# Optimization experiments

Measured on AMD Instinct MI355X. Metric: run time of the kernel, lower is better.

## Reference

```python
import jax, jax.numpy as jnp
import numpy as np

VOCAB, EMB, H, LAYERS, B, T = 50000, 128, 128, 3, 64, 512


def _lstm_dir(x, w_ih, w_hh, b_ih, b_hh, h0, c0, reverse):
    # x: [B,T,Din]; w_ih: [4H,Din]; w_hh: [4H,H]; h0,c0: [B,H]
    xg = jnp.einsum('btd,gd->btg', x, w_ih) + b_ih + b_hh  # [B,T,4H]

    def step(carry, xg_t):
        h, c = carry
        g = xg_t + h @ w_hh.T  # [B,4H]
        i, f, gg, o = jnp.split(g, 4, axis=-1)  # torch gate order i,f,g,o
        c = jax.nn.sigmoid(f) * c + jax.nn.sigmoid(i) * jnp.tanh(gg)
        h = jax.nn.sigmoid(o) * jnp.tanh(c)
        return (h, c), h

    _, hs = jax.lax.scan(step, (h0, c0), jnp.swapaxes(xg, 0, 1), reverse=reverse)
    return jnp.swapaxes(hs, 0, 1)  # [B,T,H], aligned with input time order


def _bidir_layer(x, w_ih, w_hh, b_ih, b_hh, h0, c0):
    # stacked params: leading dim 2 = (fwd, bwd)
    fwd = _lstm_dir(x, w_ih[0], w_hh[0], b_ih[0], b_hh[0], h0[0], c0[0], False)
    bwd = _lstm_dir(x, w_ih[1], w_hh[1], b_ih[1], b_hh[1], h0[1], c0[1], True)
    return jnp.concatenate([fwd, bwd], axis=-1)  # [B,T,2H]


def setup_inputs() -> dict:
    key = jax.random.key(0)
    ks = jax.random.split(key, 20)
    s = 1.0 / np.sqrt(H)
    inp = {
        'X_batch': jax.random.randint(ks[0], (B, T), 0, VOCAB),
        'emb': jax.random.normal(ks[1], (VOCAB, EMB), jnp.float32),
        'hx': jax.random.normal(ks[2], (2 * LAYERS, B, H), jnp.float32),
        'cx': jax.random.normal(ks[3], (2 * LAYERS, B, H), jnp.float32),
        'lin_w': jax.random.uniform(ks[4], (1, 2 * H), jnp.float32, -s, s),
        'lin_b': jax.random.uniform(ks[5], (1,), jnp.float32, -s, s),
    }
    k = 6
    for l in range(LAYERS):
        din = EMB if l == 0 else 2 * H
        inp[f'w_ih_{l}'] = jax.random.uniform(ks[k], (2, 4 * H, din), jnp.float32, -s, s); k += 1
        inp[f'w_hh_{l}'] = jax.random.uniform(ks[k], (2, 4 * H, H), jnp.float32, -s, s); k += 1
        inp[f'b_ih_{l}'] = jax.random.uniform(ks[k], (2, 4 * H), jnp.float32, -s, s); k += 1
        inp[f'b_hh_{l}'] = jax.random.uniform(ks[k], (2, 4 * H), jnp.float32, -s, s); k += 1
    return inp


def reference(X_batch, emb, hx, cx, lin_w, lin_b,
              w_ih_0, w_hh_0, b_ih_0, b_hh_0,
              w_ih_1, w_hh_1, b_ih_1, b_hh_1,
              w_ih_2, w_hh_2, b_ih_2, b_hh_2):
    x = emb[X_batch]  # [B,T,EMB]
    params = [(w_ih_0, w_hh_0, b_ih_0, b_hh_0),
              (w_ih_1, w_hh_1, b_ih_1, b_hh_1),
              (w_ih_2, w_hh_2, b_ih_2, b_hh_2)]
    for l, (wi, wh, bi, bh) in enumerate(params):
        x = _bidir_layer(x, wi, wh, bi, bh, hx[2 * l:2 * l + 2], cx[2 * l:2 * l + 2])
    # linear head applied to last timestep (== output[:, -1] of full linear)
    return x[:, -1] @ lin_w.T + lin_b  # [B,1]
```

## Files before the change

kernel.cpp:

```cpp
#include <hip/hip_runtime.h>
#include <hip/hip_bf16.h>
#include <stdint.h>

#define B_    64
#define T_    512
#define EMB_  128
#define H_    128
#define G4    512
#define M_    (B_ * T_)

typedef __attribute__((ext_vector_type(8))) short     short8;
typedef __attribute__((ext_vector_type(4))) float     floatx4;
typedef __attribute__((ext_vector_type(2))) _Float16  half2v;

#define GLDS(g, l) __builtin_amdgcn_global_load_lds( \
    (__attribute__((address_space(1))) void*)(g),    \
    (__attribute__((address_space(3))) void*)(l), 16, 0, 0)

__device__ __forceinline__ unsigned short f2bf_bits(float f) {
  __hip_bfloat16 h = __float2bfloat16(f);
  return *reinterpret_cast<unsigned short*>(&h);
}
__device__ __forceinline__ float bf_bits2f(unsigned short u) {
  unsigned int x = ((unsigned int)u) << 16;
  return __uint_as_float(x);
}
__device__ __forceinline__ float sigm(float x) {
  return __fdividef(1.0f, 1.0f + __expf(-x));
}
__device__ __forceinline__ float tanh_fast(float x) {
  return 1.0f - __fdividef(2.0f, __expf(2.0f * x) + 1.0f);
}

__device__ __forceinline__ unsigned int pack_f16x2(float a, float b) {
  half2v h; h.x = (_Float16)a; h.y = (_Float16)b;
  return __builtin_bit_cast(unsigned int, h);
}
__device__ __forceinline__ half2v u2h2(unsigned int u) {
  return __builtin_bit_cast(half2v, u);
}

#if __has_builtin(__builtin_amdgcn_fdot2)
__device__ __forceinline__ float fdot2(half2v a, half2v b, float c) {
  return __builtin_amdgcn_fdot2(a, b, c, false);
}
#else
__device__ __forceinline__ float fdot2(half2v a, half2v b, float c) {
  return fmaf((float)a.x, (float)b.x, fmaf((float)a.y, (float)b.y, c));
}
#endif

__device__ __forceinline__ float quad_bfly_add(float x) {
  float y = x + __int_as_float(
      __builtin_amdgcn_mov_dpp(__float_as_int(x), 0xB1, 0xF, 0xF, true));
  return y + __int_as_float(
      __builtin_amdgcn_mov_dpp(__float_as_int(y), 0x4E, 0xF, 0xF, true));
}

__device__ __forceinline__ void barrier_lds_only() {
  __asm__ __volatile__("s_waitcnt lgkmcnt(0)\n\ts_barrier" ::: "memory");
}

__device__ __forceinline__ void  store_xg(float* p, float v)  { *p = v; }
__device__ __forceinline__ void  store_xg(unsigned short* p, float v) { *p = f2bf_bits(v); }
__device__ __forceinline__ float load_xg(const float* p)  { return *p; }
__device__ __forceinline__ float load_xg(const unsigned short* p) { return bf_bits2f(*p); }

__global__ void k_gather(const int* __restrict__ X, const float* __restrict__ emb,
                         unsigned short* __restrict__ x0) {
  int i = blockIdx.x * 256 + threadIdx.x;
  int row = i >> 5, c4 = i & 31;
  float4 v = ((const float4*)emb)[(size_t)X[row] * 32 + c4];
  ushort4 o;
  o.x = f2bf_bits(v.x); o.y = f2bf_bits(v.y); o.z = f2bf_bits(v.z); o.w = f2bf_bits(v.w);
  ((ushort4*)x0)[i] = o;
}

__global__ void k_prep(const float* __restrict__ w, const float* __restrict__ bi,
                       const float* __restrict__ bh, unsigned short* __restrict__ wb,
                       float* __restrict__ bias, int nw) {
  int i = blockIdx.x * blockDim.x + threadIdx.x;
  int stride = gridDim.x * blockDim.x;
  for (int k = i; k < nw; k += stride) wb[k] = f2bf_bits(w[k]);
  for (int k = i; k < 2 * G4; k += stride) bias[k] = bi[k] + bh[k];
}

__global__ void k_prep_whh(const float* __restrict__ Whh, unsigned int* __restrict__ wf) {
  int i = blockIdx.x * 256 + threadIdx.x;
  int dir = i >> 15;
  int t2  = i & 0x7FFF;
  int jq  = t2 >> 11;
  int t3  = t2 & 0x7FF;
  int ts  = t3 >> 2;
  int q   = t3 & 3;
  int d   = jq * 4 + q;
  int g   = d >> 4;
  int jj  = d & 15;
  int lane = ts & 63, wave = ts >> 6;
  int p = lane & 3, ul = lane >> 2;
  int u = wave * 16 + ul;
  int k = 32 * p + 2 * jj;
  const float* wr = Whh + ((size_t)dir * G4 + g * H_ + u) * H_ + k;
  wf[i] = pack_f16x2(wr[0], wr[1]);
}

template <typename XG_T>
__global__ __launch_bounds__(256, 2) void k_gemm(
    const unsigned short* __restrict__ A,
    const unsigned short* __restrict__ W,
    const float* __restrict__ bias,
    XG_T* __restrict__ xg,
    int K) {
  __shared__ unsigned short sA[128 * 32];
  __shared__ unsigned short sB[128 * 32];
  const int tid  = threadIdx.x;
  const int lane = tid & 63;
  const int wave = tid >> 6;
  const int mt = blockIdx.x, nt = blockIdx.y, dir = blockIdx.z;
  const size_t Arow0 = (size_t)mt * 128;
  const int    Ncol0 = nt * 128;
  const unsigned short* Wd = W + (size_t)dir * G4 * K;

  const int srow = tid >> 2;
  const int qlog = (tid & 3) ^ ((tid >> 4) & 3);
  auto ldsA0 = (__attribute__((address_space(3))) void*)(sA + wave * 512);
  auto ldsA1 = (__attribute__((address_space(3))) void*)(sA + 2048 + wave * 512);
  auto ldsB0 = (__attribute__((address_space(3))) void*)(sB + wave * 512);
  auto ldsB1 = (__attribute__((address_space(3))) void*)(sB + 2048 + wave * 512);

  floatx4 acc[4][4];
#pragma unroll
  for (int i = 0; i < 4; ++i)
#pragma unroll
    for (int j = 0; j < 4; ++j) acc[i][j] = (floatx4)0.0f;

  const int wrow = (wave >> 1) * 64, wcol = (wave & 1) * 64;
  const int frow = lane & 15;
  const int fq   = lane >> 4;

  for (int kt = 0; kt < K; kt += 32) {
    const unsigned short* gA0 = A  + (Arow0 + srow) * (size_t)K + kt + qlog * 8;
    const unsigned short* gB0 = Wd + (size_t)(Ncol0 + srow) * K + kt + qlog * 8;
    GLDS(gA0, ldsA0);
    GLDS(gA0 + (size_t)64 * K, ldsA1);
    GLDS(gB0, ldsB0);
    GLDS(gB0 + (size_t)64 * K, ldsB1);
    __syncthreads();

    short8 af[4], bf[4];
#pragma unroll
    for (int i = 0; i < 4; ++i) {
      int r  = wrow + 16 * i + frow;
      int rn = wcol + 16 * i + frow;
      af[i] = *(const short8*)(sA + r  * 32 + ((fq ^ ((r  >> 2) & 3)) * 8));
      bf[i] = *(const short8*)(sB + rn * 32 + ((fq ^ ((rn >> 2) & 3)) * 8));
    }
#pragma unroll
    for (int i = 0; i < 4; ++i)
#pragma unroll
      for (int j = 0; j < 4; ++j)
        acc[i][j] = __builtin_amdgcn_mfma_f32_16x16x32_bf16(af[i], bf[j], acc[i][j], 0, 0, 0);
    __syncthreads();
  }

  const int r0 = (lane >> 4) * 4;
  const int cc = lane & 15;
  XG_T* xgd = xg + (size_t)dir * M_ * G4;
#pragma unroll
  for (int j = 0; j < 4; ++j) {
    int gcol = Ncol0 + wcol + 16 * j + cc;
    float bs = bias[dir * G4 + gcol];
#pragma unroll
    for (int i = 0; i < 4; ++i) {
      size_t rowb = Arow0 + wrow + 16 * i + r0;
#pragma unroll
      for (int r = 0; r < 4; ++r)
        store_xg(&xgd[(rowb + r) * G4 + gcol], acc[i][j][r] + bs);
    }
  }
}

template <typename XG_T>
__global__ __attribute__((amdgpu_flat_work_group_size(512, 512),
                          amdgpu_waves_per_eu(2, 2))) void k_scan(
    const unsigned int* __restrict__ wf,
    const float* __restrict__ hx0,
    const float* __restrict__ cx0,
    const XG_T* __restrict__ xg,
    unsigned short* __restrict__ y)
{
  const int b   = blockIdx.x & 63;
  const int dir = blockIdx.x >> 6;
  const int tid = threadIdx.x;
  const int lane = tid & 63;
  const int wave = tid >> 6;
  const int p  = lane & 3;
  const int ul = lane >> 2;
  const int u  = wave * 16 + ul;

  __shared__ __align__(16) unsigned short h16[2][128];

  uint4 wv[16];
  const uint4* wfv = (const uint4*)wf;
#pragma unroll
  for (int i = 0; i < 16; ++i) wv[i] = wfv[(dir * 16 + i) * 512 + tid];

  float c = cx0[(size_t)dir * B_ * H_ + b * H_ + u];
  if (p == 0) {
    float h0 = hx0[(size_t)dir * B_ * H_ + b * H_ + u];
    h16[0][u] = (unsigned short)(pack_f16x2(h0, 0.0f) & 0xFFFF);
  }

  const XG_T* xgb = xg + ((size_t)dir * M_ + (size_t)b * T_) * G4;
  const intptr_t xstep = dir ? -(intptr_t)G4 : (intptr_t)G4;
  const XG_T* xrow0 = xgb + (dir ? (size_t)(T_ - 1) * G4 : 0) + p * H_ + u;
  float xp0 = load_xg(xrow0);
  float xp1 = load_xg(xrow0 + xstep);
  const XG_T* xld = xrow0 + 2 * xstep;

  unsigned short* yp = y + ((size_t)b * T_ + (dir ? T_ - 1 : 0)) * (2 * H_)
                         + dir * H_ + u;
  const intptr_t ystep = dir ? -(intptr_t)(2 * H_) : (intptr_t)(2 * H_);

  __syncthreads();

  auto dots = [&](int par, float xv, float& g0, float& g1, float& g2, float& g3) {
    const uint4* hv4 = (const uint4*)&h16[par][0];
    uint4 h0v = hv4[4 * p + 0], h1v = hv4[4 * p + 1];
    uint4 h2v = hv4[4 * p + 2], h3v = hv4[4 * p + 3];
    half2v hh[16] = {
      u2h2(h0v.x), u2h2(h0v.y), u2h2(h0v.z), u2h2(h0v.w),
      u2h2(h1v.x), u2h2(h1v.y), u2h2(h1v.z), u2h2(h1v.w),
      u2h2(h2v.x), u2h2(h2v.y), u2h2(h2v.z), u2h2(h2v.w),
      u2h2(h3v.x), u2h2(h3v.y), u2h2(h3v.z), u2h2(h3v.w)};
    g0 = 0; g1 = 0; g2 = 0; g3 = 0;
#pragma unroll
    for (int j = 0; j < 16; ++j) {
      g0 = fdot2(u2h2(((const unsigned int*)&wv[(0 * 16 + j) >> 2])[(0 * 16 + j) & 3]), hh[j], g0);
      g1 = fdot2(u2h2(((const unsigned int*)&wv[(1 * 16 + j) >> 2])[(1 * 16 + j) & 3]), hh[j], g1);
      g2 = fdot2(u2h2(((const unsigned int*)&wv[(2 * 16 + j) >> 2])[(2 * 16 + j) & 3]), hh[j], g2);
      g3 = fdot2(u2h2(((const unsigned int*)&wv[(3 * 16 + j) >> 2])[(3 * 16 + j) & 3]), hh[j], g3);
    }
    g0 += (p == 0) ? xv : 0.0f;
    g1 += (p == 1) ? xv : 0.0f;
    g2 += (p == 2) ? xv : 0.0f;
    g3 += (p == 3) ? xv : 0.0f;
  };

  auto finish = [&](int par, float g0, float g1, float g2, float g3) {
    g0 = quad_bfly_add(g0);
    g1 = quad_bfly_add(g1);
    g2 = quad_bfly_add(g2);
    g3 = quad_bfly_add(g3);
    float iv = sigm(g0), fv = sigm(g1), gv = tanh_fast(g2), ov = sigm(g3);
    c = fmaf(fv, c, iv * gv);
    float h = ov * tanh_fast(c);
    if (p == 0) {
      h16[par ^ 1][u] = (unsigned short)(pack_f16x2(h, 0.0f) & 0xFFFF);
      *yp = f2bf_bits(h);
    }
    yp += ystep;
    barrier_lds_only();
  };

  for (int t = 0; t < T_; t += 2) {
    float a0, a1, a2, a3;
    dots(0, xp0, a0, a1, a2, a3);
    xp0 = (t + 2 < T_) ? load_xg(xld) : 0.0f;
    xld += xstep;
    finish(0, a0, a1, a2, a3);
    dots(1, xp1, a0, a1, a2, a3);
    xp1 = (t + 3 < T_) ? load_xg(xld) : 0.0f;
    xld += xstep;
    finish(1, a0, a1, a2, a3);
  }
}

__global__ void k_head(const unsigned short* __restrict__ y2, const float* __restrict__ lw,
                       const float* __restrict__ lb, float* __restrict__ out) {
  int b = blockIdx.x, l = threadIdx.x;
  const unsigned short* row = y2 + ((size_t)b * T_ + (T_ - 1)) * (2 * H_);
  float s = 0;
#pragma unroll
  for (int k = 0; k < 4; ++k) s += bf_bits2f(row[l + 64 * k]) * lw[l + 64 * k];
#pragma unroll
  for (int off = 32; off > 0; off >>= 1) s += __shfl_down(s, off);
  if (l == 0) out[b] = s + lb[0];
}

template <typename XG_T>
static inline void run_layers(const unsigned int* const* wfs,
                              const unsigned short* x0,
                              unsigned short* y0, unsigned short* y1, unsigned short* y2,
                              const unsigned short* wb0, const unsigned short* wb1,
                              const unsigned short* wb2,
                              const float* bias0, const float* bias1, const float* bias2,
                              const float* hx, const float* cx,
                              XG_T* xg, hipStream_t stream) {
  dim3 gg(M_ / 128, G4 / 128, 2);
  k_gemm<XG_T><<<gg, 256, 0, stream>>>(x0, wb0, bias0, xg, EMB_);
  k_scan<XG_T><<<128, 512, 0, stream>>>(wfs[0], hx, cx, xg, y0);
  k_gemm<XG_T><<<gg, 256, 0, stream>>>(y0, wb1, bias1, xg, 2 * H_);
  k_scan<XG_T><<<128, 512, 0, stream>>>(wfs[1], hx + 2 * B_ * H_, cx + 2 * B_ * H_, xg, y1);
  k_gemm<XG_T><<<gg, 256, 0, stream>>>(y1, wb2, bias2, xg, 2 * H_);
  k_scan<XG_T><<<128, 512, 0, stream>>>(wfs[2], hx + 4 * B_ * H_, cx + 4 * B_ * H_, xg, y2);
}

extern "C" void kernel_launch(void* const* d_in, const int* in_sizes, int n_in,
                              void* d_out, int out_size, void* d_ws, size_t ws_size,
                              hipStream_t stream) {
  const int*   X   = (const int*)d_in[0];
  const float* emb = (const float*)d_in[1];
  const float* hx  = (const float*)d_in[2];
  const float* cx  = (const float*)d_in[3];
  const float* lw  = (const float*)d_in[4];
  const float* lb  = (const float*)d_in[5];
  const float* w_ih[3] = {(const float*)d_in[6],  (const float*)d_in[10], (const float*)d_in[14]};
  const float* w_hh[3] = {(const float*)d_in[7],  (const float*)d_in[11], (const float*)d_in[15]};
  const float* b_ih[3] = {(const float*)d_in[8],  (const float*)d_in[12], (const float*)d_in[16]};
  const float* b_hh[3] = {(const float*)d_in[9],  (const float*)d_in[13], (const float*)d_in[17]};
  float* out = (float*)d_out;

  char* ws = (char*)d_ws;
  size_t off = 0;
  auto carve = [&](size_t bytes) {
    char* p = ws + off;
    off = (off + bytes + 255) & ~(size_t)255;
    return p;
  };
  unsigned short* x0  = (unsigned short*)carve((size_t)M_ * EMB_ * 2);
  unsigned short* y0  = (unsigned short*)carve((size_t)M_ * 2 * H_ * 2);
  unsigned short* y1  = (unsigned short*)carve((size_t)M_ * 2 * H_ * 2);
  unsigned short* y2  = (unsigned short*)carve((size_t)M_ * 2 * H_ * 2);
  unsigned short* wb0 = (unsigned short*)carve((size_t)2 * G4 * EMB_ * 2);
  unsigned short* wb1 = (unsigned short*)carve((size_t)2 * G4 * 2 * H_ * 2);
  unsigned short* wb2 = (unsigned short*)carve((size_t)2 * G4 * 2 * H_ * 2);
  float* bias0 = (float*)carve(2 * G4 * 4);
  float* bias1 = (float*)carve(2 * G4 * 4);
  float* bias2 = (float*)carve(2 * G4 * 4);
  unsigned int* wf0 = (unsigned int*)carve((size_t)65536 * 4);
  unsigned int* wf1 = (unsigned int*)carve((size_t)65536 * 4);
  unsigned int* wf2 = (unsigned int*)carve((size_t)65536 * 4);
  const size_t xg_f32_bytes = (size_t)2 * M_ * G4 * 4;
  const bool use_f32 = (off + xg_f32_bytes) <= ws_size;
  void* xg = carve(use_f32 ? xg_f32_bytes : xg_f32_bytes / 2);

  k_prep<<<256, 256, 0, stream>>>(w_ih[0], b_ih[0], b_hh[0], wb0, bias0, 2 * G4 * EMB_);
  k_prep<<<256, 256, 0, stream>>>(w_ih[1], b_ih[1], b_hh[1], wb1, bias1, 2 * G4 * 2 * H_);
  k_prep<<<256, 256, 0, stream>>>(w_ih[2], b_ih[2], b_hh[2], wb2, bias2, 2 * G4 * 2 * H_);
  k_prep_whh<<<256, 256, 0, stream>>>(w_hh[0], wf0);
  k_prep_whh<<<256, 256, 0, stream>>>(w_hh[1], wf1);
  k_prep_whh<<<256, 256, 0, stream>>>(w_hh[2], wf2);
  k_gather<<<(M_ * 32) / 256, 256, 0, stream>>>(X, emb, x0);

  const unsigned int* wfs[3] = {wf0, wf1, wf2};
  if (use_f32)
    run_layers<float>(wfs, x0, y0, y1, y2, wb0, wb1, wb2, bias0, bias1, bias2,
                      hx, cx, (float*)xg, stream);
  else
    run_layers<unsigned short>(wfs, x0, y0, y1, y2, wb0, wb1, wb2, bias0, bias1, bias2,
                               hx, cx, (unsigned short*)xg, stream);

  k_head<<<64, 64, 0, stream>>>(y2, lw, lb, out);
}
```

Measured before the change: 1.333 ms.

## Split recurrent dot products across lane pairs with 256-thread scan blocks

The LSTM scan kernel now uses 256 threads per block, with each hidden unit handled by 2 lanes instead of 4. Each lane keeps twice as many recurrent weights in registers (32 uint4). The cross-lane reduction drops from two DPP steps to one, and dual accumulators shorten the fdot2 dependency chains. The aim is to cut per-timestep reduction and barrier cost across fewer waves, at the price of higher register pressure and more serial work per lane; the weight repacking kernel is updated to match.

```diff
diff --git a/kernel.cpp b/kernel.cpp
--- a/kernel.cpp
+++ b/kernel.cpp
@@ -50,15 +50,14 @@
 }
 #endif
 
-__device__ __forceinline__ float quad_bfly_add(float x) {
-  float y = x + __int_as_float(
+__device__ __forceinline__ float pair_bfly_add(float x) {
+  return x + __int_as_float(
       __builtin_amdgcn_mov_dpp(__float_as_int(x), 0xB1, 0xF, 0xF, true));
-  return y + __int_as_float(
-      __builtin_amdgcn_mov_dpp(__float_as_int(y), 0x4E, 0xF, 0xF, true));
 }
 
 __device__ __forceinline__ void barrier_lds_only() {
-  __asm__ __volatile__("s_waitcnt lgkmcnt(0)\n\ts_barrier" ::: "memory");
+  __builtin_amdgcn_s_waitcnt(0xC07F);
+  __builtin_amdgcn_s_barrier();
 }
 
 __device__ __forceinline__ void  store_xg(float* p, float v)  { *p = v; }
@@ -88,18 +87,18 @@
 __global__ void k_prep_whh(const float* __restrict__ Whh, unsigned int* __restrict__ wf) {
   int i = blockIdx.x * 256 + threadIdx.x;
   int dir = i >> 15;
-  int t2  = i & 0x7FFF;
-  int jq  = t2 >> 11;
-  int t3  = t2 & 0x7FF;
-  int ts  = t3 >> 2;
-  int q   = t3 & 3;
-  int d   = jq * 4 + q;
-  int g   = d >> 4;
-  int jj  = d & 15;
-  int lane = ts & 63, wave = ts >> 6;
-  int p = lane & 3, ul = lane >> 2;
-  int u = wave * 16 + ul;
-  int k = 32 * p + 2 * jj;
+  int r   = i & 0x7FFF;
+  int i4  = r >> 10;
+  int r2  = r & 0x3FF;
+  int ts  = r2 >> 2;
+  int q   = r2 & 3;
+  int d   = i4 * 4 + q;
+  int g   = d >> 5;
+  int jj  = d & 31;
+  int lane = ts & 63, w = ts >> 6;
+  int p = lane & 1, ul = lane >> 1;
+  int u = w * 32 + ul;
+  int k = 64 * p + 2 * jj;
   const float* wr = Whh + ((size_t)dir * G4 + g * H_ + u) * H_ + k;
   wf[i] = pack_f16x2(wr[0], wr[1]);
 }
@@ -181,8 +180,8 @@
 }
 
 template <typename XG_T>
-__global__ __attribute__((amdgpu_flat_work_group_size(512, 512),
-                          amdgpu_waves_per_eu(2, 2))) void k_scan(
+__global__ __attribute__((amdgpu_flat_work_group_size(256, 256),
+                          amdgpu_waves_per_eu(1, 1))) void k_scan(
     const unsigned int* __restrict__ wf,
     const float* __restrict__ hx0,
     const float* __restrict__ cx0,
@@ -194,16 +193,16 @@
   const int tid = threadIdx.x;
   const int lane = tid & 63;
   const int wave = tid >> 6;
-  const int p  = lane & 3;
-  const int ul = lane >> 2;
-  const int u  = wave * 16 + ul;
+  const int p  = lane & 1;
+  const int ul = lane >> 1;
+  const int u  = wave * 32 + ul;
 
   __shared__ __align__(16) unsigned short h16[2][128];
 
-  uint4 wv[16];
+  uint4 wv[32];
   const uint4* wfv = (const uint4*)wf;
 #pragma unroll
-  for (int i = 0; i < 16; ++i) wv[i] = wfv[(dir * 16 + i) * 512 + tid];
+  for (int i = 0; i < 32; ++i) wv[i] = wfv[(dir * 32 + i) * 256 + tid];
 
   float c = cx0[(size_t)dir * B_ * H_ + b * H_ + u];
   if (p == 0) {
@@ -213,9 +212,11 @@
 
   const XG_T* xgb = xg + ((size_t)dir * M_ + (size_t)b * T_) * G4;
   const intptr_t xstep = dir ? -(intptr_t)G4 : (intptr_t)G4;
-  const XG_T* xrow0 = xgb + (dir ? (size_t)(T_ - 1) * G4 : 0) + p * H_ + u;
-  float xp0 = load_xg(xrow0);
-  float xp1 = load_xg(xrow0 + xstep);
+  const int o0 = (2 * p) * H_ + u;
+  const int o1 = o0 + H_;
+  const XG_T* xrow0 = xgb + (dir ? (size_t)(T_ - 1) * G4 : 0);
+  float xa0 = load_xg(xrow0 + o0), xb0 = load_xg(xrow0 + o1);
+  float xa1 = load_xg(xrow0 + xstep + o0), xb1 = load_xg(xrow0 + xstep + o1);
   const XG_T* xld = xrow0 + 2 * xstep;
 
   unsigned short* yp = y + ((size_t)b * T_ + (dir ? T_ - 1 : 0)) * (2 * H_)
@@ -224,34 +225,45 @@
 
   __syncthreads();
 
-  auto dots = [&](int par, float xv, float& g0, float& g1, float& g2, float& g3) {
+  auto dots = [&](int par, float xva, float xvb,
+                  float& g0, float& g1, float& g2, float& g3) {
     const uint4* hv4 = (const uint4*)&h16[par][0];
-    uint4 h0v = hv4[4 * p + 0], h1v = hv4[4 * p + 1];
-    uint4 h2v = hv4[4 * p + 2], h3v = hv4[4 * p + 3];
-    half2v hh[16] = {
-      u2h2(h0v.x), u2h2(h0v.y), u2h2(h0v.z), u2h2(h0v.w),
-      u2h2(h1v.x), u2h2(h1v.y), u2h2(h1v.z), u2h2(h1v.w),
-      u2h2(h2v.x), u2h2(h2v.y), u2h2(h2v.z), u2h2(h2v.w),
-      u2h2(h3v.x), u2h2(h3v.y), u2h2(h3v.z), u2h2(h3v.w)};
-    g0 = 0; g1 = 0; g2 = 0; g3 = 0;
+    uint4 hq[8];
+#pragma unroll
+    for (int i = 0; i < 8; ++i) hq[i] = hv4[8 * p + i];
+    half2v hh[32];
+#pragma unroll
+    for (int i = 0; i < 8; ++i) {
+      hh[4 * i + 0] = u2h2(hq[i].x);
+      hh[4 * i + 1] = u2h2(hq[i].y);
+      hh[4 * i + 2] = u2h2(hq[i].z);
+      hh[4 * i + 3] = u2h2(hq[i].w);
+    }
+    float A0 = 0, B0 = 0, A1 = 0, B1 = 0, A2 = 0, B2 = 0, A3 = 0, B3 = 0;
 #pragma unroll
     for (int j = 0; j < 16; ++j) {
-      g0 = fdot2(u2h2(((const unsigned int*)&wv[(0 * 16 + j) >> 2])[(0 * 16 + j) & 3]), hh[j], g0);
-      g1 = fdot2(u2h2(((const unsigned int*)&wv[(1 * 16 + j) >> 2])[(1 * 16 + j) & 3]), hh[j], g1);
-      g2 = fdot2(u2h2(((const unsigned int*)&wv[(2 * 16 + j) >> 2])[(2 * 16 + j) & 3]), hh[j], g2);
-      g3 = fdot2(u2h2(((const unsigned int*)&wv[(3 * 16 + j) >> 2])[(3 * 16 + j) & 3]), hh[j], g3);
-    }
-    g0 += (p == 0) ? xv : 0.0f;
-    g1 += (p == 1) ? xv : 0.0f;
-    g2 += (p == 2) ? xv : 0.0f;
-    g3 += (p == 3) ? xv : 0.0f;
+      int d0 = j, d1 = j + 16;
+      A0 = fdot2(u2h2(((const unsigned int*)&wv[(0 * 32 + d0) >> 2])[(0 * 32 + d0) & 3]), hh[d0], A0);
+      A1 = fdot2(u2h2(((const unsigned int*)&wv[(1 * 32 + d0) >> 2])[(1 * 32 + d0) & 3]), hh[d0], A1);
+      A2 = fdot2(u2h2(((const unsigned int*)&wv[(2 * 32 + d0) >> 2])[(2 * 32 + d0) & 3]), hh[d0], A2);
+      A3 = fdot2(u2h2(((const unsigned int*)&wv[(3 * 32 + d0) >> 2])[(3 * 32 + d0) & 3]), hh[d0], A3);
+      B0 = fdot2(u2h2(((const unsigned int*)&wv[(0 * 32 + d1) >> 2])[(0 * 32 + d1) & 3]), hh[d1], B0);
+      B1 = fdot2(u2h2(((const unsigned int*)&wv[(1 * 32 + d1) >> 2])[(1 * 32 + d1) & 3]), hh[d1], B1);
+      B2 = fdot2(u2h2(((const unsigned int*)&wv[(2 * 32 + d1) >> 2])[(2 * 32 + d1) & 3]), hh[d1], B2);
+      B3 = fdot2(u2h2(((const unsigned int*)&wv[(3 * 32 + d1) >> 2])[(3 * 32 + d1) & 3]), hh[d1], B3);
+    }
+    g0 = A0 + B0; g1 = A1 + B1; g2 = A2 + B2; g3 = A3 + B3;
+    g0 += (p == 0) ? xva : 0.0f;
+    g1 += (p == 0) ? xvb : 0.0f;
+    g2 += (p == 1) ? xva : 0.0f;
+    g3 += (p == 1) ? xvb : 0.0f;
   };
 
   auto finish = [&](int par, float g0, float g1, float g2, float g3) {
-    g0 = quad_bfly_add(g0);
-    g1 = quad_bfly_add(g1);
-    g2 = quad_bfly_add(g2);
-    g3 = quad_bfly_add(g3);
+    g0 = pair_bfly_add(g0);
+    g1 = pair_bfly_add(g1);
+    g2 = pair_bfly_add(g2);
+    g3 = pair_bfly_add(g3);
     float iv = sigm(g0), fv = sigm(g1), gv = tanh_fast(g2), ov = sigm(g3);
     c = fmaf(fv, c, iv * gv);
     float h = ov * tanh_fast(c);
@@ -264,15 +276,24 @@
   };
 
   for (int t = 0; t < T_; t += 2) {
-    float a0, a1, a2, a3;
-    dots(0, xp0, a0, a1, a2, a3);
-    xp0 = (t + 2 < T_) ? load_xg(xld) : 0.0f;
-    xld += xstep;
-    finish(0, a0, a1, a2, a3);
-    dots(1, xp1, a0, a1, a2, a3);
-    xp1 = (t + 3 < T_) ? load_xg(xld) : 0.0f;
-    xld += xstep;
-    finish(1, a0, a1, a2, a3);
+    {
+      float va = xa0, vb = xb0;
+      if (t + 2 < T_) { xa0 = load_xg(xld + o0); xb0 = load_xg(xld + o1); }
+      else            { xa0 = 0.0f; xb0 = 0.0f; }
+      xld += xstep;
+      float a0, a1, a2, a3;
+      dots(0, va, vb, a0, a1, a2, a3);
+      finish(0, a0, a1, a2, a3);
+    }
+    {
+      float va = xa1, vb = xb1;
+      if (t + 3 < T_) { xa1 = load_xg(xld + o0); xb1 = load_xg(xld + o1); }
+      else            { xa1 = 0.0f; xb1 = 0.0f; }
+      xld += xstep;
+      float a0, a1, a2, a3;
+      dots(1, va, vb, a0, a1, a2, a3);
+      finish(1, a0, a1, a2, a3);
+    }
   }
 }
 
@@ -299,11 +320,11 @@
                               XG_T* xg, hipStream_t stream) {
   dim3 gg(M_ / 128, G4 / 128, 2);
   k_gemm<XG_T><<<gg, 256, 0, stream>>>(x0, wb0, bias0, xg, EMB_);
-  k_scan<XG_T><<<128, 512, 0, stream>>>(wfs[0], hx, cx, xg, y0);
+  k_scan<XG_T><<<128, 256, 0, stream>>>(wfs[0], hx, cx, xg, y0);
   k_gemm<XG_T><<<gg, 256, 0, stream>>>(y0, wb1, bias1, xg, 2 * H_);
-  k_scan<XG_T><<<128, 512, 0, stream>>>(wfs[1], hx + 2 * B_ * H_, cx + 2 * B_ * H_, xg, y1);
+  k_scan<XG_T><<<128, 256, 0, stream>>>(wfs[1], hx + 2 * B_ * H_, cx + 2 * B_ * H_, xg, y1);
   k_gemm<XG_T><<<gg, 256, 0, stream>>>(y1, wb2, bias2, xg, 2 * H_);
-  k_scan<XG_T><<<128, 512, 0, stream>>>(wfs[2], hx + 4 * B_ * H_, cx + 4 * B_ * H_, xg, y2);
+  k_scan<XG_T><<<128, 256, 0, stream>>>(wfs[2], hx + 4 * B_ * H_, cx + 4 * B_ * H_, xg, y2);
 }
 
 extern "C" void kernel_launch(void* const* d_in, const int* in_sizes, int n_in,
```

Result: faster. 1.121 ms (-15.9%).

## Halve scan workgroup to 4 waves, each thread computing two hidden units

Applied to the files above, without the earlier changes.

The recurrent scan kernel now runs with 256 threads instead of 512. Each thread holds twice as many W_hh fragments in registers (32 uint4) and computes dot products for two hidden units, and the quad lanes pick their own unit's gates after the butterfly reduction. The W_hh repacking kernel is changed to match the new layout. The aim is a cheaper per-step barrier with fewer waves and more independent FMA chains per thread, at the cost of doubling dot-product work per thread and higher register pressure. The barrier inline asm is also swapped for builtins.

```diff
diff --git a/kernel.cpp b/kernel.cpp
--- a/kernel.cpp
+++ b/kernel.cpp
@@ -58,7 +58,8 @@
 }
 
 __device__ __forceinline__ void barrier_lds_only() {
-  __asm__ __volatile__("s_waitcnt lgkmcnt(0)\n\ts_barrier" ::: "memory");
+  __builtin_amdgcn_s_waitcnt(0xC07F);
+  __builtin_amdgcn_s_barrier();
 }
 
 __device__ __forceinline__ void  store_xg(float* p, float v)  { *p = v; }
@@ -88,17 +89,18 @@
 __global__ void k_prep_whh(const float* __restrict__ Whh, unsigned int* __restrict__ wf) {
   int i = blockIdx.x * 256 + threadIdx.x;
   int dir = i >> 15;
-  int t2  = i & 0x7FFF;
-  int jq  = t2 >> 11;
-  int t3  = t2 & 0x7FF;
-  int ts  = t3 >> 2;
-  int q   = t3 & 3;
-  int d   = jq * 4 + q;
-  int g   = d >> 4;
+  int r   = i & 0x7FFF;
+  int i4  = r >> 10;
+  int r2  = r & 0x3FF;
+  int ts  = r2 >> 2;
+  int qq  = r2 & 3;
+  int d   = i4 * 4 + qq;
+  int U   = d >> 6;
+  int g   = (d >> 4) & 3;
   int jj  = d & 15;
-  int lane = ts & 63, wave = ts >> 6;
-  int p = lane & 3, ul = lane >> 2;
-  int u = wave * 16 + ul;
+  int lane = ts & 63, w = ts >> 6;
+  int p = lane & 3, q = lane >> 2;
+  int u = w * 32 + U * 16 + q;
   int k = 32 * p + 2 * jj;
   const float* wr = Whh + ((size_t)dir * G4 + g * H_ + u) * H_ + k;
   wf[i] = pack_f16x2(wr[0], wr[1]);
@@ -181,8 +183,8 @@
 }
 
 template <typename XG_T>
-__global__ __attribute__((amdgpu_flat_work_group_size(512, 512),
-                          amdgpu_waves_per_eu(2, 2))) void k_scan(
+__global__ __attribute__((amdgpu_flat_work_group_size(256, 256),
+                          amdgpu_waves_per_eu(1, 1))) void k_scan(
     const unsigned int* __restrict__ wf,
     const float* __restrict__ hx0,
     const float* __restrict__ cx0,
@@ -195,27 +197,30 @@
   const int lane = tid & 63;
   const int wave = tid >> 6;
   const int p  = lane & 3;
-  const int ul = lane >> 2;
-  const int u  = wave * 16 + ul;
+  const int q  = lane >> 2;
+  const int uA = wave * 32 + q;
+  const int uB = uA + 16;
+  const int u  = (p >> 1) ? uB : uA;
 
   __shared__ __align__(16) unsigned short h16[2][128];
 
-  uint4 wv[16];
+  uint4 wv[32];
   const uint4* wfv = (const uint4*)wf;
 #pragma unroll
-  for (int i = 0; i < 16; ++i) wv[i] = wfv[(dir * 16 + i) * 512 + tid];
+  for (int i = 0; i < 32; ++i) wv[i] = wfv[(dir * 32 + i) * 256 + tid];
 
   float c = cx0[(size_t)dir * B_ * H_ + b * H_ + u];
-  if (p == 0) {
+  if ((p & 1) == 0) {
     float h0 = hx0[(size_t)dir * B_ * H_ + b * H_ + u];
     h16[0][u] = (unsigned short)(pack_f16x2(h0, 0.0f) & 0xFFFF);
   }
 
   const XG_T* xgb = xg + ((size_t)dir * M_ + (size_t)b * T_) * G4;
   const intptr_t xstep = dir ? -(intptr_t)G4 : (intptr_t)G4;
-  const XG_T* xrow0 = xgb + (dir ? (size_t)(T_ - 1) * G4 : 0) + p * H_ + u;
-  float xp0 = load_xg(xrow0);
-  float xp1 = load_xg(xrow0 + xstep);
+  const int oA = p * H_ + uA, oB = oA + 16;
+  const XG_T* xrow0 = xgb + (dir ? (size_t)(T_ - 1) * G4 : 0);
+  float xa0 = load_xg(xrow0 + oA), xb0 = load_xg(xrow0 + oB);
+  float xa1 = load_xg(xrow0 + xstep + oA), xb1 = load_xg(xrow0 + xstep + oB);
   const XG_T* xld = xrow0 + 2 * xstep;
 
   unsigned short* yp = y + ((size_t)b * T_ + (dir ? T_ - 1 : 0)) * (2 * H_)
@@ -224,7 +229,9 @@
 
   __syncthreads();
 
-  auto dots = [&](int par, float xv, float& g0, float& g1, float& g2, float& g3) {
+#define WVD(d) u2h2(((const unsigned int*)&wv[(d) >> 2])[(d) & 3])
+
+  auto dots = [&](int par, float xa, float xb, float* s) {
     const uint4* hv4 = (const uint4*)&h16[par][0];
     uint4 h0v = hv4[4 * p + 0], h1v = hv4[4 * p + 1];
     uint4 h2v = hv4[4 * p + 2], h3v = hv4[4 * p + 3];
@@ -233,29 +240,37 @@
       u2h2(h1v.x), u2h2(h1v.y), u2h2(h1v.z), u2h2(h1v.w),
       u2h2(h2v.x), u2h2(h2v.y), u2h2(h2v.z), u2h2(h2v.w),
       u2h2(h3v.x), u2h2(h3v.y), u2h2(h3v.z), u2h2(h3v.w)};
-    g0 = 0; g1 = 0; g2 = 0; g3 = 0;
-#pragma unroll
-    for (int j = 0; j < 16; ++j) {
-      g0 = fdot2(u2h2(((const unsigned int*)&wv[(0 * 16 + j) >> 2])[(0 * 16 + j) & 3]), hh[j], g0);
-      g1 = fdot2(u2h2(((const unsigned int*)&wv[(1 * 16 + j) >> 2])[(1 * 16 + j) & 3]), hh[j], g1);
-      g2 = fdot2(u2h2(((const unsigned int*)&wv[(2 * 16 + j) >> 2])[(2 * 16 + j) & 3]), hh[j], g2);
-      g3 = fdot2(u2h2(((const unsigned int*)&wv[(3 * 16 + j) >> 2])[(3 * 16 + j) & 3]), hh[j], g3);
-    }
-    g0 += (p == 0) ? xv : 0.0f;
-    g1 += (p == 1) ? xv : 0.0f;
-    g2 += (p == 2) ? xv : 0.0f;
-    g3 += (p == 3) ? xv : 0.0f;
+    float A0 = 0, A1 = 0, A2 = 0, A3 = 0, B0 = 0, B1 = 0, B2 = 0, B3 = 0;
+#pragma unroll
+    for (int jj = 0; jj < 16; ++jj) {
+      A0 = fdot2(WVD(0 * 16 + jj), hh[jj], A0);
+      A1 = fdot2(WVD(1 * 16 + jj), hh[jj], A1);
+      A2 = fdot2(WVD(2 * 16 + jj), hh[jj], A2);
+      A3 = fdot2(WVD(3 * 16 + jj), hh[jj], A3);
+      B0 = fdot2(WVD(64 + 0 * 16 + jj), hh[jj], B0);
+      B1 = fdot2(WVD(64 + 1 * 16 + jj), hh[jj], B1);
+      B2 = fdot2(WVD(64 + 2 * 16 + jj), hh[jj], B2);
+      B3 = fdot2(WVD(64 + 3 * 16 + jj), hh[jj], B3);
+    }
+    A0 += (p == 0) ? xa : 0.0f;  B0 += (p == 0) ? xb : 0.0f;
+    A1 += (p == 1) ? xa : 0.0f;  B1 += (p == 1) ? xb : 0.0f;
+    A2 += (p == 2) ? xa : 0.0f;  B2 += (p == 2) ? xb : 0.0f;
+    A3 += (p == 3) ? xa : 0.0f;  B3 += (p == 3) ? xb : 0.0f;
+    s[0] = A0; s[1] = A1; s[2] = A2; s[3] = A3;
+    s[4] = B0; s[5] = B1; s[6] = B2; s[7] = B3;
   };
 
-  auto finish = [&](int par, float g0, float g1, float g2, float g3) {
-    g0 = quad_bfly_add(g0);
-    g1 = quad_bfly_add(g1);
-    g2 = quad_bfly_add(g2);
-    g3 = quad_bfly_add(g3);
+  auto finish = [&](int par, float* s) {
+#pragma unroll
+    for (int i = 0; i < 8; ++i) s[i] = quad_bfly_add(s[i]);
+    float g0 = (p >> 1) ? s[4] : s[0];
+    float g1 = (p >> 1) ? s[5] : s[1];
+    float g2 = (p >> 1) ? s[6] : s[2];
+    float g3 = (p >> 1) ? s[7] : s[3];
     float iv = sigm(g0), fv = sigm(g1), gv = tanh_fast(g2), ov = sigm(g3);
     c = fmaf(fv, c, iv * gv);
     float h = ov * tanh_fast(c);
-    if (p == 0) {
+    if ((p & 1) == 0) {
       h16[par ^ 1][u] = (unsigned short)(pack_f16x2(h, 0.0f) & 0xFFFF);
       *yp = f2bf_bits(h);
     }
@@ -264,16 +279,26 @@
   };
 
   for (int t = 0; t < T_; t += 2) {
-    float a0, a1, a2, a3;
-    dots(0, xp0, a0, a1, a2, a3);
-    xp0 = (t + 2 < T_) ? load_xg(xld) : 0.0f;
-    xld += xstep;
-    finish(0, a0, a1, a2, a3);
-    dots(1, xp1, a0, a1, a2, a3);
-    xp1 = (t + 3 < T_) ? load_xg(xld) : 0.0f;
-    xld += xstep;
-    finish(1, a0, a1, a2, a3);
+    {
+      float va = xa0, vb = xb0;
+      if (t + 2 < T_) { xa0 = load_xg(xld + oA); xb0 = load_xg(xld + oB); }
+      else            { xa0 = 0.0f; xb0 = 0.0f; }
+      xld += xstep;
+      float s[8];
+      dots(0, va, vb, s);
+      finish(0, s);
+    }
+    {
+      float va = xa1, vb = xb1;
+      if (t + 3 < T_) { xa1 = load_xg(xld + oA); xb1 = load_xg(xld + oB); }
+      else            { xa1 = 0.0f; xb1 = 0.0f; }
+      xld += xstep;
+      float s[8];
+      dots(1, va, vb, s);
+      finish(1, s);
+    }
   }
+#undef WVD
 }
 
 __global__ void k_head(const unsigned short* __restrict__ y2, const float* __restrict__ lw,
@@ -299,11 +324,11 @@
                               XG_T* xg, hipStream_t stream) {
   dim3 gg(M_ / 128, G4 / 128, 2);
   k_gemm<XG_T><<<gg, 256, 0, stream>>>(x0, wb0, bias0, xg, EMB_);
-  k_scan<XG_T><<<128, 512, 0, stream>>>(wfs[0], hx, cx, xg, y0);
+  k_scan<XG_T><<<128, 256, 0, stream>>>(wfs[0], hx, cx, xg, y0);
   k_gemm<XG_T><<<gg, 256, 0, stream>>>(y0, wb1, bias1, xg, 2 * H_);
-  k_scan<XG_T><<<128, 512, 0, stream>>>(wfs[1], hx + 2 * B_ * H_, cx + 2 * B_ * H_, xg, y1);
+  k_scan<XG_T><<<128, 256, 0, stream>>>(wfs[1], hx + 2 * B_ * H_, cx + 2 * B_ * H_, xg, y1);
   k_gemm<XG_T><<<gg, 256, 0, stream>>>(y1, wb2, bias2, xg, 2 * H_);
-  k_scan<XG_T><<<128, 512, 0, stream>>>(wfs[2], hx + 4 * B_ * H_, cx + 4 * B_ * H_, xg, y2);
+  k_scan<XG_T><<<128, 256, 0, stream>>>(wfs[2], hx + 4 * B_ * H_, cx + 4 * B_ * H_, xg, y2);
 }
 
 extern "C" void kernel_launch(void* const* d_in, const int* in_sizes, int n_in,
```

Measured after the change: 1.148 ms. 13.9% less time.
